# Optimization experiments

Hardware: AMD Instinct MI355X
Metric: run time of the kernel (lower is better)

Reference implementation:

```python
import jax, jax.numpy as jnp
import numpy as np

ALPHA = 0.2  # LeakyReLU negative slope
NEG_INF = -1e12


def setup_inputs() -> dict:
    key = jax.random.key(0)
    k1, k2, k3, k4 = jax.random.split(key, 4)
    B, N, F_in, F_out = 8, 4096, 128, 64
    inp = jax.random.normal(k1, (B, N, F_in), dtype=jnp.float32)
    adj = jax.random.randint(k2, (B, N, N), 0, 2, dtype=jnp.int32)
    # xavier-uniform-ish init for W, a
    W = jax.random.normal(k3, (F_in, F_out), dtype=jnp.float32) * (2.0 / (F_in + F_out)) ** 0.5
    a = jax.random.normal(k4, (2 * F_out, 1), dtype=jnp.float32) * (2.0 / (2 * F_out + 1)) ** 0.5
    return {"inp": inp, "adj": adj, "W": W, "a": a}


def reference(inp, adj, W, a):
    # inp: [B,N,F_in], adj: [B,N,N] int, W: [F_in,F_out], a: [2*F_out,1]
    F_out = W.shape[1]
    h = jnp.einsum('bnf,fo->bno', inp, W)          # [B,N,F_out]
    a1 = a[:F_out, 0]                              # [F_out]
    a2 = a[F_out:, 0]                              # [F_out]
    # e[b,i,j] = leakyrelu(h_i . a1 + h_j . a2)  (== concat([h_i,h_j]) @ a)
    s1 = h @ a1                                    # [B,N]
    s2 = h @ a2                                    # [B,N]
    e = s1[:, :, None] + s2[:, None, :]            # [B,N,N]
    e = jnp.where(e > 0, e, ALPHA * e)             # LeakyReLU
    att = jnp.where(adj > 0, e, NEG_INF)
    att = jax.nn.softmax(att, axis=-1)             # [B,N,N]
    # dropout p=0.0 -> identity
    h_prime = jnp.einsum('bij,bjo->bio', att, h)   # [B,N,F_out]
    return jax.nn.elu(h_prime)
```

## Files before the change

### kernel.cpp

```cpp
#include <hip/hip_runtime.h>
#include <hip/hip_bf16.h>
#include <hip/hip_fp16.h>
#include <cstdint>

typedef __attribute__((ext_vector_type(8))) short short8;
typedef __attribute__((ext_vector_type(4))) float floatx4;

#define LEAKY_ALPHA 0.2f

__device__ __forceinline__ unsigned short f2bf_rne(float f) {
    unsigned u = __float_as_uint(f);
    unsigned r = u + 0x7FFFu + ((u >> 16) & 1u);
    return (unsigned short)(r >> 16);
}

__device__ __forceinline__ unsigned pk2bf(float lo, float hi) {
    union { __hip_bfloat162 b; unsigned u; } c;
    c.b = __float22bfloat162_rn(make_float2(lo, hi));
    return c.u;
}

__device__ __forceinline__ float2 h2f2(unsigned w) {
    union { unsigned u; __half2 h; } c; c.u = w;
    return __half22float2(c.h);
}


__global__ __launch_bounds__(256) void k_h(const float* __restrict__ inp,
                                           const float* __restrict__ W,
                                           const float* __restrict__ a,
                                           unsigned short* __restrict__ hT,
                                           float2* __restrict__ e1,
                                           __half2* __restrict__ e2h) {
    __shared__ float hs[64][65];
    const int tid  = threadIdx.x;
    const int wv   = tid >> 6;
    const int lane = tid & 63;
    const int blk  = blockIdx.x;
    const int b     = blk >> 6;
    const int ibase = (blk & 63) * 64;

    const float a1 = a[lane];
    const float a2 = a[64 + lane];

    for (int rr = 0; rr < 16; ++rr) {
        const int rloc = wv * 16 + rr;
        const int row  = ibase + rloc;
        const float* ip = inp + ((size_t)(b * 4096 + row)) * 128;
        float acc = 0.f;
        #pragma unroll
        for (int f = 0; f < 128; f += 4) {
            float4 v = *(const float4*)(ip + f);
            acc += v.x * W[(f + 0) * 64 + lane];
            acc += v.y * W[(f + 1) * 64 + lane];
            acc += v.z * W[(f + 2) * 64 + lane];
            acc += v.w * W[(f + 3) * 64 + lane];
        }
        hs[rloc][lane] = acc;
        float r1 = acc * a1;
        float r2 = acc * a2;
        #pragma unroll
        for (int off = 32; off > 0; off >>= 1) {
            r1 += __shfl_xor(r1, off);
            r2 += __shfl_xor(r2, off);
        }
        if (lane == 0) {
            e1[b * 4096 + row]  = make_float2(__expf(r1), __expf(LEAKY_ALPHA * r1));
            e2h[b * 4096 + row] = __floats2half2_rn(__expf(r2), __expf(LEAKY_ALPHA * r2));
        }
    }
    __syncthreads();

    const int o    = tid & 63;
    const int half = tid >> 6;
    const int tl   = half >> 1;
    const int nco  = (half & 1) * 16;
    unsigned pk[8];
    #pragma unroll
    for (int s = 0; s < 16; s += 2) {
        const int n0 = nco + s, n1 = nco + s + 1;
        const int c0 = 4 * (n0 & 7) + (n0 >> 3);
        const int c1 = 4 * (n1 & 7) + (n1 >> 3);
        unsigned lo = f2bf_rne(hs[tl * 32 + c0][o]);
        unsigned hi = f2bf_rne(hs[tl * 32 + c1][o]);
        pk[s >> 1] = lo | (hi << 16);
    }
    const int tile = (ibase >> 5) + tl;
    unsigned short* dst = hT + (((size_t)b * 128 + tile) * 64 + o) * 32 + nco;
    *(int4*)(dst)     = *(int4*)&pk[0];
    *(int4*)(dst + 8) = *(int4*)&pk[4];
}

__global__ __launch_bounds__(256, 4) void k_fused(const int* __restrict__ adj,
                                                  const unsigned short* __restrict__ hT,
                                                  const float2* __restrict__ e1g,
                                                  const __half2* __restrict__ e2hg,
                                                  float* __restrict__ out) {
    __shared__ unsigned long long mask64[32][17][4];
    __shared__ unsigned e2su[4096];

    const int tid   = threadIdx.x;
    const int b     = blockIdx.x >> 7;
    const int rtile = blockIdx.x & 127;
    const int wv    = tid >> 6;
    const int lane  = tid & 63;

    {
        const unsigned* src = (const unsigned*)(e2hg + b * 4096);
        #pragma unroll
        for (int t = 0; t < 4; ++t) {
            const int c0 = tid * 16 + t * 4;
            const int4 raw = *(const int4*)(src + c0);
            const int base = (c0 & ~31) + ((c0 & 31) >> 2);
            e2su[base +  0] = (unsigned)raw.x;
            e2su[base +  8] = (unsigned)raw.y;
            e2su[base + 16] = (unsigned)raw.z;
            e2su[base + 24] = (unsigned)raw.w;
        }
    }

    const int* abase = adj + ((size_t)(b * 4096 + rtile * 32)) * 4096;

#define PACK_ONE(LR, GRP)                                                      \
    {                                                                          \
        const int4 v = *(const int4*)(abase + (size_t)(LR) * 4096              \
                                      + (GRP) * 256 + lane * 4);               \
        const unsigned long long b0 = __ballot(v.x > 0);                       \
        const unsigned long long b1 = __ballot(v.y > 0);                       \
        const unsigned long long b2 = __ballot(v.z > 0);                       \
        const unsigned long long b3 = __ballot(v.w > 0);                       \
        if (lane == 0) {                                                       \
            ulonglong2* d = (ulonglong2*)&mask64[LR][GRP][0];                  \
            ulonglong2 t0; t0.x = b0; t0.y = b1;                               \
            ulonglong2 t1; t1.x = b2; t1.y = b3;                               \
            d[0] = t0; d[1] = t1;                                              \
        }                                                                      \
    }

#define PACK2(GA, GB)                                                          \
    _Pragma("unroll 2")                                                        \
    for (int r = 0; r < 8; ++r) {                                              \
        const int lr = wv * 8 + r;                                             \
        PACK_ONE(lr, (GA));                                                    \
        PACK_ONE(lr, (GB));                                                    \
    }

    PACK2(0, 8);

    const int jhalf = wv >> 1;
    const int m     = lane & 15;
    const int kh    = lane >> 4;
    const int rl    = (wv & 1) * 16 + m;
    const int rbase = rtile * 32 + (wv & 1) * 16;
    const int row   = rbase + m;

    const float2 E1 = e1g[b * 4096 + row];
    const float E1p = E1.x, E1n = E1.y;
    const int jb0 = jhalf * 2048 + kh * 8;

    const unsigned short* hbase =
        hT + (((size_t)b * 128 + jhalf * 64) * 64 + m) * 32 + kh * 8;
    const unsigned short* hrow0 = hbase;
    const unsigned short* hrow1 = hbase + 512;
    const unsigned short* hrow2 = hbase + 1024;
    const unsigned short* hrow3 = hbase + 1536;

    floatx4 acc0 = (floatx4){0.f,0.f,0.f,0.f};
    floatx4 acc1 = (floatx4){0.f,0.f,0.f,0.f};
    floatx4 acc2 = (floatx4){0.f,0.f,0.f,0.f};
    floatx4 acc3 = (floatx4){0.f,0.f,0.f,0.f};
    float lsum = 0.f;

    short8 rb0_0, rb1_0, rb2_0, rb3_0, rb0_1, rb1_1, rb2_1, rb3_1;
    rb0_0 = *(const short8*)(hrow0);         rb1_0 = *(const short8*)(hrow1);
    rb2_0 = *(const short8*)(hrow2);         rb3_0 = *(const short8*)(hrow3);
    rb0_1 = *(const short8*)(hrow0 + 2048);  rb1_1 = *(const short8*)(hrow1 + 2048);
    rb2_1 = *(const short8*)(hrow2 + 2048);  rb3_1 = *(const short8*)(hrow3 + 2048);

    __syncthreads();

#define GAT_COL(WRD, T)                                                        \
    {                                                                          \
        const float2 ef = h2f2((unsigned)(WRD));                               \
        const float P  = E1p * ef.x;                                           \
        const float Nn = E1n * ef.y;                                           \
        float p = (P > 1.0f) ? P : Nn;                                         \
        p = ((mb >> (T)) & 1u) ? p : 0.0f;                                     \
        psum += p;                                                             \
        pv[T] = p;                                                             \
    }

#define GAT_STEP(SL, STEPIDX)                                                  \
    do {                                                                       \
        const short8 cb0 = rb0_##SL, cb1 = rb1_##SL;                           \
        const short8 cb2 = rb2_##SL, cb3 = rb3_##SL;                           \
        const int pstep = ((STEPIDX) + 2) & 63;         \
        const int poff = pstep * 2048;                         \
        rb0_##SL = *(const short8*)(hrow0 + poff);                             \
        rb1_##SL = *(const short8*)(hrow1 + poff);                             \
        rb2_##SL = *(const short8*)(hrow2 + poff);                             \
        rb3_##SL = *(const short8*)(hrow3 + poff);                             \
        const int soff = jb0 + (STEPIDX) * 32;                                 \
        const int4 eA = *(const int4*)&e2su[soff];                             \
        const int4 eB = *(const int4*)&e2su[soff + 4];                         \
        const unsigned mb = (unsigned)(Mcur >> (8 * ((STEPIDX) & 7))) & 0xffu; \
        float pv[8];                                                           \
        float psum = 0.f;                                                      \
        GAT_COL(eA.x, 0) GAT_COL(eA.y, 1) GAT_COL(eA.z, 2) GAT_COL(eA.w, 3)    \
        GAT_COL(eB.x, 4) GAT_COL(eB.y, 5) GAT_COL(eB.z, 6) GAT_COL(eB.w, 7)    \
        lsum += psum;                                                          \
        int4 ai;                                                               \
        ai.x = pk2bf(pv[0], pv[1]); ai.y = pk2bf(pv[2], pv[3]);                \
        ai.z = pk2bf(pv[4], pv[5]); ai.w = pk2bf(pv[6], pv[7]);                \
        union { int4 i; short8 s; } cc; cc.i = ai;                             \
        const short8 af = cc.s;                                                \
        acc0 = __builtin_amdgcn_mfma_f32_16x16x32_bf16(af, cb0, acc0, 0,0,0);  \
        acc1 = __builtin_amdgcn_mfma_f32_16x16x32_bf16(af, cb1, acc1, 0,0,0);  \
        acc2 = __builtin_amdgcn_mfma_f32_16x16x32_bf16(af, cb2, acc2, 0,0,0);  \
        acc3 = __builtin_amdgcn_mfma_f32_16x16x32_bf16(af, cb3, acc3, 0,0,0);  \
    } while (0)

    #pragma unroll 1
    for (int p = 0; p < 8; ++p) {
        const unsigned long long Mcur =
            *(const unsigned long long*)&mask64[rl][jhalf * 8 + p][kh];
        #pragma unroll
        for (int q = 0; q < 4; ++q) {
            GAT_STEP(0, p * 8 + 2 * q);
            GAT_STEP(1, p * 8 + 2 * q + 1);
        }
        if (p < 7) {
            PACK2(p + 1, p + 9);
        }
        __syncthreads();
    }
#undef GAT_STEP
#undef GAT_COL
#undef PACK2
#undef PACK_ONE

    lsum += __shfl_xor(lsum, 16);
    lsum += __shfl_xor(lsum, 32);

    floatx4 accs[4] = {acc0, acc1, acc2, acc3};

    float* accb = (float*)&mask64[0][0][0];
    float* lb   = accb + 2 * 64 * 17;

    if (wv >= 2) {
        #pragma unroll
        for (int f = 0; f < 4; ++f)
            #pragma unroll
            for (int r = 0; r < 4; ++r)
                accb[(wv - 2) * 64 * 17 + lane * 17 + f * 4 + r] = accs[f][r];
        lb[(wv - 2) * 64 + lane] = lsum;
    }
    __syncthreads();
    if (wv < 2) {
        const float ltot = lsum + lb[wv * 64 + lane];
        #pragma unroll
        for (int f = 0; f < 4; ++f) {
            #pragma unroll
            for (int r = 0; r < 4; ++r) {
                float v = accs[f][r] + accb[wv * 64 * 17 + lane * 17 + f * 4 + r];
                const int drow = (lane >> 4) * 4 + r;
                const float lr = __shfl(ltot, drow);
                const float hp = v / lr;
                const float o  = (hp > 0.f) ? hp : (__expf(hp) - 1.f);
                out[((size_t)(b * 4096 + rbase + drow)) * 64 + f * 16 + (lane & 15)] = o;
            }
        }
    }
}

extern "C" void kernel_launch(void* const* d_in, const int* in_sizes, int n_in,
                              void* d_out, int out_size, void* d_ws, size_t ws_size,
                              hipStream_t stream) {
    const float* inp = (const float*)d_in[0];
    const int*   adj = (const int*)d_in[1];
    const float* W   = (const float*)d_in[2];
    const float* a   = (const float*)d_in[3];
    float* out = (float*)d_out;

    unsigned short* hT = (unsigned short*)d_ws;
    float2*  e1  = (float2*)((char*)d_ws + (size_t)4 * 1024 * 1024);
    __half2* e2h = (__half2*)((char*)d_ws + (size_t)4 * 1024 * 1024 + 262144);

    k_h<<<512, 256, 0, stream>>>(inp, W, a, hT, e1, e2h);
    k_fused<<<1024, 256, 0, stream>>>(adj, hT, e1, e2h, out);
}
```

Before: 902.1 us.

## Pack full adjacency mask upfront with nontemporal loads and drop per-step barriers

Moves all adjacency-to-bitmask packing ahead of the attention/MFMA loop. Previously, packing of the next column groups was interleaved with each gather step, with a block barrier every iteration. The adjacency reads now use nontemporal loads, the mask padding column is dropped, and the eight in-loop __syncthreads are removed in favour of one barrier before the reduction. This removes per-iteration synchronisation and simplifies the loop. In exchange, adjacency memory traffic no longer overlaps with compute inside a block, so it relies on other resident blocks to hide that latency.

```diff
diff --git a/kernel.cpp b/kernel.cpp
--- a/kernel.cpp
+++ b/kernel.cpp
@@ -5,6 +5,7 @@
 
 typedef __attribute__((ext_vector_type(8))) short short8;
 typedef __attribute__((ext_vector_type(4))) float floatx4;
+typedef __attribute__((ext_vector_type(4))) int   intx4;
 
 #define LEAKY_ALPHA 0.2f
 
@@ -96,7 +97,7 @@
                                                   const float2* __restrict__ e1g,
                                                   const __half2* __restrict__ e2hg,
                                                   float* __restrict__ out) {
-    __shared__ unsigned long long mask64[32][17][4];
+    __shared__ unsigned long long mask64[32][16][4];
     __shared__ unsigned e2su[4096];
 
     const int tid   = threadIdx.x;
@@ -119,33 +120,27 @@
         }
     }
 
-    const int* abase = adj + ((size_t)(b * 4096 + rtile * 32)) * 4096;
-
-#define PACK_ONE(LR, GRP)                                                      \
-    {                                                                          \
-        const int4 v = *(const int4*)(abase + (size_t)(LR) * 4096              \
-                                      + (GRP) * 256 + lane * 4);               \
-        const unsigned long long b0 = __ballot(v.x > 0);                       \
-        const unsigned long long b1 = __ballot(v.y > 0);                       \
-        const unsigned long long b2 = __ballot(v.z > 0);                       \
-        const unsigned long long b3 = __ballot(v.w > 0);                       \
-        if (lane == 0) {                                                       \
-            ulonglong2* d = (ulonglong2*)&mask64[LR][GRP][0];                  \
-            ulonglong2 t0; t0.x = b0; t0.y = b1;                               \
-            ulonglong2 t1; t1.x = b2; t1.y = b3;                               \
-            d[0] = t0; d[1] = t1;                                              \
-        }                                                                      \
-    }
-
-#define PACK2(GA, GB)                                                          \
-    _Pragma("unroll 2")                                                        \
-    for (int r = 0; r < 8; ++r) {                                              \
-        const int lr = wv * 8 + r;                                             \
-        PACK_ONE(lr, (GA));                                                    \
-        PACK_ONE(lr, (GB));                                                    \
-    }
-
-    PACK2(0, 8);
+    {
+        const int* abase = adj + ((size_t)(b * 4096 + rtile * 32)) * 4096;
+        for (int r = 0; r < 8; ++r) {
+            const int lr = wv * 8 + r;
+            const int* prow = abase + (size_t)lr * 4096 + lane * 4;
+            #pragma unroll 4
+            for (int g = 0; g < 16; ++g) {
+                const intx4 v = __builtin_nontemporal_load((const intx4*)(prow + g * 256));
+                const unsigned long long b0 = __ballot(v.x > 0);
+                const unsigned long long b1 = __ballot(v.y > 0);
+                const unsigned long long b2 = __ballot(v.z > 0);
+                const unsigned long long b3 = __ballot(v.w > 0);
+                if (lane == 0) {
+                    ulonglong2* d = (ulonglong2*)&mask64[lr][g][0];
+                    ulonglong2 t0; t0.x = b0; t0.y = b1;
+                    ulonglong2 t1; t1.x = b2; t1.y = b3;
+                    d[0] = t0; d[1] = t1;
+                }
+            }
+        }
+    }
 
     const int jhalf = wv >> 1;
     const int m     = lane & 15;
@@ -229,15 +224,9 @@
             GAT_STEP(0, p * 8 + 2 * q);
             GAT_STEP(1, p * 8 + 2 * q + 1);
         }
-        if (p < 7) {
-            PACK2(p + 1, p + 9);
-        }
-        __syncthreads();
     }
 #undef GAT_STEP
 #undef GAT_COL
-#undef PACK2
-#undef PACK_ONE
 
     lsum += __shfl_xor(lsum, 16);
     lsum += __shfl_xor(lsum, 32);
@@ -247,6 +236,7 @@
     float* accb = (float*)&mask64[0][0][0];
     float* lb   = accb + 2 * 64 * 17;
 
+    __syncthreads();
     if (wv >= 2) {
         #pragma unroll
         for (int f = 0; f < 4; ++f)
```

Result: faster. 791.9 us (-12.2%).
